# Optimization experiments

Measured on AMD Instinct MI355X. Metric: run time of the kernel, lower is better.

Reference implementation:

```python
import jax, jax.numpy as jnp
import numpy as np

N = 100000   # num nodes
E = 1000000  # num edges (avg degree 10)
F = 64       # feat_dim
H = 64       # hidden_dim
O = 16       # output_dim


def setup_inputs() -> dict:
    key = jax.random.key(0)
    ks = jax.random.split(key, 14)
    s = 0.05
    return {
        "real_feature": jax.random.normal(ks[0], (N, F), jnp.float32),
        "imag_feature": jax.random.normal(ks[1], (N, F), jnp.float32),
        "edge_weight_sym": jax.random.uniform(ks[2], (E,), jnp.float32),
        "exp_weight_q": jnp.float32(1.0),
        "edge_entropy": jax.random.uniform(ks[3], (E,), jnp.float32),
        "edge_cluster_coefficient": jax.random.uniform(ks[4], (E,), jnp.float32),
        "W1": jax.random.normal(ks[5], (H, F), jnp.float32) * s,
        "b1": jax.random.normal(ks[6], (H,), jnp.float32) * s,
        "W2": jax.random.normal(ks[7], (H, H), jnp.float32) * s,
        "b2": jax.random.normal(ks[8], (H,), jnp.float32) * s,
        "W3": jax.random.normal(ks[9], (O, 2 * H), jnp.float32) * s,
        "b3": jax.random.normal(ks[10], (O,), jnp.float32) * s,
        "row": jax.random.randint(ks[11], (E,), 0, N, jnp.int32),
        "col": jax.random.randint(ks[12], (E,), 0, N, jnp.int32),
    }


def reference(real_feature, imag_feature, edge_weight_sym, exp_weight_q,
              edge_entropy, edge_cluster_coefficient,
              W1, b1, W2, b2, W3, b3, row, col):
    # structure-encoded complex edge weights (soft_label is None branch)
    se = edge_entropy + edge_cluster_coefficient            # [E]
    phase = exp_weight_q * se
    wr = edge_weight_sym * jnp.cos(phase)                   # real adj values
    wi = edge_weight_sym * jnp.sin(phase)                   # imag adj values

    def spmm(w, x):
        # out[row] += w * x[col]  == torch.mm(sparse_coo(indices, w), x)
        return jax.ops.segment_sum(w[:, None] * x[col], row, num_segments=N)

    def layer(xr, xi, W, b):
        rr = spmm(wr, xr)   # real_adj @ real
        ii = spmm(wi, xi)   # imag_adj @ imag
        ir = spmm(wi, xr)   # imag_adj @ real
        ri = spmm(wr, xi)   # real_adj @ imag
        # fc(rr) - fc(ii): bias cancels; fc(ir) + fc(ri): bias doubles
        out_r = (rr - ii) @ W.T
        out_i = (ir + ri) @ W.T + 2.0 * b
        # ComReLU: ReLU applied to real and imag parts independently
        return jax.nn.relu(out_r), jax.nn.relu(out_i)

    r1, i1 = layer(real_feature, imag_feature, W1, b1)  # dropout=eval -> identity
    r2, i2 = layer(r1, i1, W2, b2)
    x = jnp.concatenate([r2, i2], axis=-1)              # [N, 2H]
    return x @ W3.T + b3                                # [N, O]
```

## Files before the change

### kernel.cpp

```cpp
#include <hip/hip_runtime.h>
#include <hip/hip_fp16.h>


typedef __attribute__((ext_vector_type(8))) _Float16 half8;
typedef __attribute__((ext_vector_type(4))) float f32x4;

#define LW 72
#define LW3 136
#define NBKTMAX 400
#define CAP 16

__device__ __forceinline__ unsigned short hbits(float f) {
  return __half_as_ushort(__float2half_rn(f));
}
__device__ __forceinline__ unsigned packh2(float a, float b) {
  return ((unsigned)hbits(b) << 16) | (unsigned)hbits(a);
}
__device__ __forceinline__ float2 unpackh2(unsigned u) {
  __half2 h = *reinterpret_cast<__half2*>(&u);
  return __half22float2(h);
}

__global__ void prep_k(const float4* __restrict__ xr, const float4* __restrict__ xi,
                       uint4* __restrict__ xc, int n4,
                       const int* __restrict__ row, int* __restrict__ cnt, int E) {
  int i = blockIdx.x * 256 + threadIdx.x;
  if (i < E) atomicAdd(&cnt[row[i]], 1);
  if (i < n4) {
    float4 r = xr[i], m = xi[i];
    xc[i] = make_uint4(packh2(r.x, m.x), packh2(r.y, m.y),
                       packh2(r.z, m.z), packh2(r.w, m.w));
  }
}

__global__ void offs_k(const int* __restrict__ cnt, int* __restrict__ offs,
                       int* __restrict__ total,
                       int* __restrict__ gcur, int N, int nch) {
  int ch = blockIdx.x * 4 + (threadIdx.x >> 6);
  if (ch >= nch) return;
  int lane = threadIdx.x & 63;
  int n0 = ch * 256 + lane * 4;
  int v0 = 0, v1 = 0, v2 = 0, v3 = 0;
  if (n0 + 3 < N) {
    int4 v = *(const int4*)&cnt[n0];
    v0 = v.x; v1 = v.y; v2 = v.z; v3 = v.w;
  } else {
    if (n0 + 0 < N) v0 = cnt[n0 + 0];
    if (n0 + 1 < N) v1 = cnt[n0 + 1];
    if (n0 + 2 < N) v2 = cnt[n0 + 2];
    if (n0 + 3 < N) v3 = cnt[n0 + 3];
  }
  int s = v0 + v1 + v2 + v3;
  int x = s;
#pragma unroll
  for (int d = 1; d < 64; d <<= 1) {
    int t = __shfl_up(x, d);
    if (lane >= d) x += t;
  }
  int excl = x - s;
  int wtot = __shfl(x, 63);
  int base = 0;
  if (lane == 63) base = atomicAdd(total, wtot);
  base = __shfl(base, 63);
  if (lane == 0) gcur[ch] = base;
  int e0 = base + excl;
  if (n0 + 0 < N) offs[n0 + 0] = e0;
  if (n0 + 1 < N) offs[n0 + 1] = e0 + v0;
  if (n0 + 2 < N) offs[n0 + 2] = e0 + v0 + v1;
  if (n0 + 3 < N) offs[n0 + 3] = e0 + v0 + v1 + v2;
}

__global__ void __launch_bounds__(256) bin_k(
    const int* __restrict__ row, const int* __restrict__ col,
    const float* __restrict__ wsym, const float* __restrict__ qp,
    const float* __restrict__ ent, const float* __restrict__ cc,
    int* __restrict__ gcur, uint2* __restrict__ tmp,
    int E, int nbkt, int ntiles) {
  __shared__ int lcnt[NBKTMAX];
  __shared__ int lgp[NBKTMAX];
  __shared__ uint2 lbuf[NBKTMAX * CAP];
  const float q = qp[0];
  for (int t = blockIdx.x; t < ntiles; t += gridDim.x) {
    for (int i = threadIdx.x; i < nbkt; i += 256) lcnt[i] = 0;
    __syncthreads();
    int base = t * 2048;
#pragma unroll
    for (int j = 0; j < 8; ++j) {
      int e = base + j * 256 + threadIdx.x;
      if (e < E) {
        float ph = q * (ent[e] + cc[e]);
        float s = __sinf(ph), c = __cosf(ph);
        float w = wsym[e];
        int r = row[e];
        uint2 rec = make_uint2((unsigned)col[e] | ((unsigned)(r & 255) << 24),
                               packh2(w * c, w * s));
        int b = r >> 8;
        int pos = atomicAdd(&lcnt[b], 1);
        if (pos < CAP) lbuf[b * CAP + pos] = rec;
        else {
          int gp = atomicAdd(&gcur[b], 1);
          tmp[gp] = rec;
        }
      }
    }
    __syncthreads();
    for (int b = threadIdx.x; b < nbkt; b += 256) {
      int c = lcnt[b];
      if (c > CAP) c = CAP;
      lgp[b] = (c > 0) ? atomicAdd(&gcur[b], c) : 0;
    }
    __syncthreads();
    int slots = nbkt * CAP;
    for (int i = threadIdx.x; i < slots; i += 256) {
      int b = i >> 4, j = i & (CAP - 1);
      int c = lcnt[b];
      if (c > CAP) c = CAP;
      if (j < c) tmp[lgp[b] + j] = lbuf[i];
    }
    __syncthreads();
  }
}

__global__ void __launch_bounds__(256) fine_k(
    const uint2* __restrict__ tmp, const int* __restrict__ offs,
    const int* __restrict__ cnt, uint2* __restrict__ crec, int N) {
  __shared__ int ls[256];
  __shared__ int fill[256];
  int first = blockIdx.x << 8;
  int nlast = first + 256;
  if (nlast > N) nlast = N;
  nlast -= 1;
  int beg = offs[first];
  int end = offs[nlast] + cnt[nlast];
  int tid = threadIdx.x;
  int n = first + tid;
  ls[tid] = (n <= nlast) ? (offs[n] - beg) : 0;
  fill[tid] = 0;
  __syncthreads();
  for (int i = beg + tid; i < end; i += 256) {
    uint2 r = tmp[i];
    int loc = (int)(r.x >> 24);
    unsigned c = r.x & 0xFFFFFFu;
    int pos = beg + ls[loc] + atomicAdd(&fill[loc], 1);
    crec[pos] = make_uint2(c | ((unsigned)(loc & 15) << 28), r.y);
  }
}

struct AccRI {
  f32x4 r[4], i[4];
};

__device__ __forceinline__ AccRI spmm_gemv(
    const unsigned* __restrict__ tbl,
    const int* __restrict__ offs, const int* __restrict__ cnt,
    const uint2* __restrict__ crec,
    const _Float16* __restrict__ sW,
    _Float16* __restrict__ s_ar, _Float16* __restrict__ s_ai,
    int n0, int N, int lane) {
  const int c16 = lane & 15, q16 = lane >> 4;
  int nlast = n0 + 15;
  if (nlast >= N) nlast = N - 1;
  int ebeg = __builtin_amdgcn_readfirstlane(offs[n0]);
  int eend = __builtin_amdgcn_readfirstlane(offs[nlast] + cnt[nlast]);
  int total = eend - ebeg;

  uint2 rA[16], rB[16];
  unsigned vA[16], vB[16];
  float ar = 0.f, ai = 0.f;
  int ni = 0;

#define LOADRECS(base_, recs_)                                        \
  do {                                                                \
    if ((base_) + 16 <= total) {                                      \
      _Pragma("unroll") for (int j = 0; j < 16; ++j)                  \
          (recs_)[j] = crec[ebeg + (base_) + j];                      \
    } else {                                                          \
      _Pragma("unroll") for (int j = 0; j < 16; ++j) {                \
        int idx_ = ((base_) + j < total) ? ebeg + (base_) + j : ebeg; \
        (recs_)[j] = crec[idx_];                                      \
      }                                                               \
    }                                                                 \
  } while (0)

#define ISSUEV(recs_, v_)                                                  \
  do {                                                                     \
    _Pragma("unroll") for (int j = 0; j < 16; ++j)                         \
        (v_)[j] = tbl[(unsigned)((recs_)[j].x & 0x0FFFFFFFu) * 64u + lane]; \
  } while (0)

#define FLUSHTO(nrel_)                      \
  while (ni < (nrel_)) {                    \
    s_ar[ni * LW + lane] = (_Float16)ar;    \
    s_ai[ni * LW + lane] = (_Float16)ai;    \
    ar = 0.f;                               \
    ai = 0.f;                               \
    ++ni;                                   \
  }

#define CONSUME(recs_, v_, base_)                               \
  do {                                                          \
    _Pragma("unroll") for (int j = 0; j < 16; ++j) {            \
      if ((base_) + j >= total) break;                          \
      int nrel_ = (recs_)[j].x >> 28;                           \
      FLUSHTO(nrel_);                                           \
      float2 val_ = unpackh2((v_)[j]);                          \
      float2 wv_ = unpackh2((recs_)[j].y);                      \
      ar = fmaf(wv_.x, val_.x, fmaf(-wv_.y, val_.y, ar));       \
      ai = fmaf(wv_.y, val_.x, fmaf(wv_.x, val_.y, ai));        \
    }                                                           \
  } while (0)

  int nbatch = (total + 15) >> 4;
  if (nbatch > 0) {
    LOADRECS(0, rA);
    ISSUEV(rA, vA);
    if (nbatch > 1) LOADRECS(16, rB);
    for (int b = 0; b < nbatch; b += 2) {
      if (b + 1 < nbatch) ISSUEV(rB, vB);
      CONSUME(rA, vA, b * 16);
      if (b + 2 < nbatch) LOADRECS((b + 2) * 16, rA);
      if (b + 1 < nbatch) {
        if (b + 2 < nbatch) ISSUEV(rA, vA);
        CONSUME(rB, vB, (b + 1) * 16);
        if (b + 3 < nbatch) LOADRECS((b + 3) * 16, rB);
      }
    }
  }
  FLUSHTO(16);
#undef LOADRECS
#undef ISSUEV
#undef FLUSHTO
#undef CONSUME

  half8 a_r[2], a_i[2];
#pragma unroll
  for (int ks = 0; ks < 2; ++ks) {
    int off = c16 * LW + ks * 32 + q16 * 8;
    a_r[ks] = *(const half8*)&s_ar[off];
    a_i[ks] = *(const half8*)&s_ai[off];
  }
  AccRI acc;
#pragma unroll
  for (int nt = 0; nt < 4; ++nt) {
    acc.r[nt] = (f32x4){0.f, 0.f, 0.f, 0.f};
    acc.i[nt] = (f32x4){0.f, 0.f, 0.f, 0.f};
  }
#pragma unroll
  for (int nt = 0; nt < 4; ++nt)
#pragma unroll
    for (int ks = 0; ks < 2; ++ks) {
      half8 b = *(const half8*)&sW[(nt * 16 + c16) * LW + ks * 32 + q16 * 8];
      acc.r[nt] = __builtin_amdgcn_mfma_f32_16x16x32_f16(a_r[ks], b, acc.r[nt], 0, 0, 0);
      acc.i[nt] = __builtin_amdgcn_mfma_f32_16x16x32_f16(a_i[ks], b, acc.i[nt], 0, 0, 0);
    }
  return acc;
}

__global__ void __launch_bounds__(512, 6) layer1_k(
    const unsigned* __restrict__ xc,
    const int* __restrict__ offs, const int* __restrict__ cnt,
    const uint2* __restrict__ crec,
    const float* __restrict__ W, const float* __restrict__ bias,
    unsigned* __restrict__ Hc, int N) {
  __shared__ __align__(16) _Float16 sW[64 * LW];
  __shared__ __align__(16) _Float16 s_act[8][2][16 * LW];
  for (int i = threadIdx.x; i < 64 * 64; i += 512)
    sW[(i >> 6) * LW + (i & 63)] = (_Float16)W[i];
  __syncthreads();
  const int w = threadIdx.x >> 6, lane = threadIdx.x & 63;
  const int c16 = lane & 15, q16 = lane >> 4;
  int n0 = (blockIdx.x * 8 + w) * 16;
  if (n0 >= N) return;
  float bl[4];
#pragma unroll
  for (int nt = 0; nt < 4; ++nt) bl[nt] = 2.f * bias[nt * 16 + c16];

  AccRI acc = spmm_gemv(xc, offs, cnt, crec, sW,
                        &s_act[w][0][0], &s_act[w][1][0], n0, N, lane);
#pragma unroll
  for (int nt = 0; nt < 4; ++nt)
#pragma unroll
    for (int r = 0; r < 4; ++r) {
      int node = n0 + q16 * 4 + r;
      if (node < N) {
        float hr = fmaxf(acc.r[nt][r], 0.f);
        float hi = fmaxf(acc.i[nt][r] + bl[nt], 0.f);
        Hc[(unsigned)node * 64u + nt * 16 + c16] = packh2(hr, hi);
      }
    }
}

__global__ void __launch_bounds__(512, 6) layer2_k(
    const unsigned* __restrict__ Hc,
    const int* __restrict__ offs, const int* __restrict__ cnt,
    const uint2* __restrict__ crec,
    const float* __restrict__ W2, const float* __restrict__ b2,
    const float* __restrict__ W3, const float* __restrict__ b3,
    float* __restrict__ out, int N) {
  __shared__ __align__(16) _Float16 sW[64 * LW];
  __shared__ __align__(16) _Float16 sW3p[16 * LW3];
  __shared__ __align__(16) _Float16 s_act[8][2][16 * LW];
  for (int i = threadIdx.x; i < 64 * 64; i += 512)
    sW[(i >> 6) * LW + (i & 63)] = (_Float16)W2[i];
  for (int i = threadIdx.x; i < 16 * 128; i += 512) {
    int o = i >> 7, kp = i & 127;
    sW3p[o * LW3 + kp] = (_Float16)W3[o * 128 + (kp >> 1) + 64 * (kp & 1)];
  }
  __syncthreads();
  const int w = threadIdx.x >> 6, lane = threadIdx.x & 63;
  const int c16 = lane & 15, q16 = lane >> 4;
  int n0 = (blockIdx.x * 8 + w) * 16;
  if (n0 >= N) return;
  float bl[4];
#pragma unroll
  for (int nt = 0; nt < 4; ++nt) bl[nt] = 2.f * b2[nt * 16 + c16];
  const float b3v = b3[c16];

  AccRI acc = spmm_gemv(Hc, offs, cnt, crec, sW,
                        &s_act[w][0][0], &s_act[w][1][0], n0, N, lane);

  unsigned* pb = (unsigned*)&s_act[w][0][0];
#pragma unroll
  for (int nt = 0; nt < 4; ++nt)
#pragma unroll
    for (int r = 0; r < 4; ++r) {
      float hr = fmaxf(acc.r[nt][r], 0.f);
      float hi = fmaxf(acc.i[nt][r] + bl[nt], 0.f);
      pb[(q16 * 4 + r) * 68 + nt * 16 + c16] = packh2(hr, hi);
    }
  f32x4 po = {0.f, 0.f, 0.f, 0.f};
#pragma unroll
  for (int ks = 0; ks < 4; ++ks) {
    half8 a = *(const half8*)((const _Float16*)pb + c16 * LW3 + ks * 32 + q16 * 8);
    half8 b = *(const half8*)&sW3p[c16 * LW3 + ks * 32 + q16 * 8];
    po = __builtin_amdgcn_mfma_f32_16x16x32_f16(a, b, po, 0, 0, 0);
  }
#pragma unroll
  for (int r = 0; r < 4; ++r) {
    int node = n0 + q16 * 4 + r;
    if (node < N) out[(unsigned)node * 16u + c16] = po[r] + b3v;
  }
}

extern "C" void kernel_launch(void* const* d_in, const int* in_sizes, int n_in,
                              void* d_out, int out_size, void* d_ws, size_t ws_size,
                              hipStream_t stream) {
  const float* xr   = (const float*)d_in[0];
  const float* xi   = (const float*)d_in[1];
  const float* wsym = (const float*)d_in[2];
  const float* qp   = (const float*)d_in[3];
  const float* ent  = (const float*)d_in[4];
  const float* cc   = (const float*)d_in[5];
  const float* W1   = (const float*)d_in[6];
  const float* b1   = (const float*)d_in[7];
  const float* W2   = (const float*)d_in[8];
  const float* b2   = (const float*)d_in[9];
  const float* W3   = (const float*)d_in[10];
  const float* b3   = (const float*)d_in[11];
  const int*   row  = (const int*)d_in[12];
  const int*   col  = (const int*)d_in[13];
  const int N = in_sizes[0] / 64;
  const int E = in_sizes[2];
  float* out = (float*)d_out;

  char* ws = (char*)d_ws;
  size_t off = 0;
  auto alloc = [&](size_t bytes) -> void* {
    void* p = ws + off;
    off += (bytes + 255) & ~(size_t)255;
    return p;
  };
  int*      cnt    = (int*)alloc((size_t)N * 4);
  int*      offs   = (int*)alloc((size_t)N * 4);
  int*      total  = (int*)alloc(256);
  int*      gcur   = (int*)alloc((size_t)NBKTMAX * 4);
  uint2*    crec   = (uint2*)alloc((size_t)E * 8);
  unsigned* xc     = (unsigned*)alloc((size_t)N * 64 * 4);
  unsigned* Hc     = (unsigned*)alloc((size_t)N * 64 * 4);
  uint2*    tmp    = (uint2*)Hc;

  hipMemsetAsync(cnt, 0, (size_t)N * 4, stream);
  hipMemsetAsync(total, 0, 256, stream);
  int n4 = N * 64 / 4;
  int npre = (n4 > E ? n4 : E);
  prep_k<<<(npre + 255) / 256, 256, 0, stream>>>((const float4*)xr, (const float4*)xi,
                                                 (uint4*)xc, n4, row, cnt, E);
  int nch = (N + 255) / 256;
  offs_k<<<(nch + 3) / 4, 256, 0, stream>>>(cnt, offs, total, gcur, N, nch);
  int ntiles = (E + 2047) / 2048;
  bin_k<<<ntiles, 256, 0, stream>>>(row, col, wsym, qp, ent, cc, gcur, tmp,
                                    E, nch, ntiles);
  fine_k<<<nch, 256, 0, stream>>>(tmp, offs, cnt, crec, N);
  int nb = (N + 127) / 128;
  layer1_k<<<nb, 512, 0, stream>>>(xc, offs, cnt, crec, W1, b1, Hc, N);
  layer2_k<<<nb, 512, 0, stream>>>(Hc, offs, cnt, crec, W2, b2, W3, b3, out, N);
}
```

Measured before the change: 198.6 us.

## Replace per-node global histogram with chunk histogram and in-block per-node counting

Per-node degree counting with global atomics is replaced by a shared-memory histogram over 256-node chunks plus a single-block chunk scan. Per-node offsets are now computed inside fine_k via a local count and block scan, and the CSR offsets array gains an N+1 sentinel so the cnt array goes away. The fp16 feature packing moves into bin_k, removing the prep kernel and the N-sized memset. This cuts global atomic contention and kernel count, at the cost of an extra pass over tmp in fine_k and a serial single-block scan.

```diff
diff --git a/kernel.cpp b/kernel.cpp
--- a/kernel.cpp
+++ b/kernel.cpp
@@ -21,61 +21,52 @@
   return __half22float2(h);
 }
 
-__global__ void prep_k(const float4* __restrict__ xr, const float4* __restrict__ xi,
-                       uint4* __restrict__ xc, int n4,
-                       const int* __restrict__ row, int* __restrict__ cnt, int E) {
-  int i = blockIdx.x * 256 + threadIdx.x;
-  if (i < E) atomicAdd(&cnt[row[i]], 1);
-  if (i < n4) {
-    float4 r = xr[i], m = xi[i];
-    xc[i] = make_uint4(packh2(r.x, m.x), packh2(r.y, m.y),
-                       packh2(r.z, m.z), packh2(r.w, m.w));
-  }
-}
-
-__global__ void offs_k(const int* __restrict__ cnt, int* __restrict__ offs,
-                       int* __restrict__ total,
-                       int* __restrict__ gcur, int N, int nch) {
-  int ch = blockIdx.x * 4 + (threadIdx.x >> 6);
-  if (ch >= nch) return;
-  int lane = threadIdx.x & 63;
-  int n0 = ch * 256 + lane * 4;
-  int v0 = 0, v1 = 0, v2 = 0, v3 = 0;
-  if (n0 + 3 < N) {
-    int4 v = *(const int4*)&cnt[n0];
-    v0 = v.x; v1 = v.y; v2 = v.z; v3 = v.w;
-  } else {
-    if (n0 + 0 < N) v0 = cnt[n0 + 0];
-    if (n0 + 1 < N) v1 = cnt[n0 + 1];
-    if (n0 + 2 < N) v2 = cnt[n0 + 2];
-    if (n0 + 3 < N) v3 = cnt[n0 + 3];
-  }
-  int s = v0 + v1 + v2 + v3;
-  int x = s;
-#pragma unroll
-  for (int d = 1; d < 64; d <<= 1) {
-    int t = __shfl_up(x, d);
-    if (lane >= d) x += t;
-  }
-  int excl = x - s;
-  int wtot = __shfl(x, 63);
-  int base = 0;
-  if (lane == 63) base = atomicAdd(total, wtot);
-  base = __shfl(base, 63);
-  if (lane == 0) gcur[ch] = base;
-  int e0 = base + excl;
-  if (n0 + 0 < N) offs[n0 + 0] = e0;
-  if (n0 + 1 < N) offs[n0 + 1] = e0 + v0;
-  if (n0 + 2 < N) offs[n0 + 2] = e0 + v0 + v1;
-  if (n0 + 3 < N) offs[n0 + 3] = e0 + v0 + v1 + v2;
+__global__ void hist_k(const int* __restrict__ row, int* __restrict__ chcnt,
+                       int E, int nch) {
+  __shared__ int h[NBKTMAX];
+  for (int i = threadIdx.x; i < nch; i += 256) h[i] = 0;
+  __syncthreads();
+  for (int e = blockIdx.x * 256 + threadIdx.x; e < E; e += gridDim.x * 256)
+    atomicAdd(&h[row[e] >> 8], 1);
+  __syncthreads();
+  for (int i = threadIdx.x; i < nch; i += 256)
+    if (h[i]) atomicAdd(&chcnt[i], h[i]);
+}
+
+__global__ void cscan_k(const int* __restrict__ chcnt, int* __restrict__ chbase,
+                        int* __restrict__ gcur, int nch, int E) {
+  __shared__ int buf[512];
+  int t = threadIdx.x;
+  int v = (t < nch) ? chcnt[t] : 0;
+  buf[t] = v;
+  __syncthreads();
+  for (int d = 1; d < 512; d <<= 1) {
+    int y = (t >= d) ? buf[t - d] : 0;
+    __syncthreads();
+    buf[t] += y;
+    __syncthreads();
+  }
+  int excl = buf[t] - v;
+  if (t < nch) {
+    chbase[t] = excl;
+    gcur[t] = excl;
+  }
+  if (t == nch) chbase[nch] = E;
 }
 
 __global__ void __launch_bounds__(256) bin_k(
+    const float4* __restrict__ xr, const float4* __restrict__ xi,
+    uint4* __restrict__ xc, int n4,
     const int* __restrict__ row, const int* __restrict__ col,
     const float* __restrict__ wsym, const float* __restrict__ qp,
     const float* __restrict__ ent, const float* __restrict__ cc,
     int* __restrict__ gcur, uint2* __restrict__ tmp,
     int E, int nbkt, int ntiles) {
+  for (int i = blockIdx.x * 256 + threadIdx.x; i < n4; i += gridDim.x * 256) {
+    float4 r = xr[i], m = xi[i];
+    xc[i] = make_uint4(packh2(r.x, m.x), packh2(r.y, m.y),
+                       packh2(r.z, m.z), packh2(r.w, m.w));
+  }
   __shared__ int lcnt[NBKTMAX];
   __shared__ int lgp[NBKTMAX];
   __shared__ uint2 lbuf[NBKTMAX * CAP];
@@ -122,20 +113,37 @@
 }
 
 __global__ void __launch_bounds__(256) fine_k(
-    const uint2* __restrict__ tmp, const int* __restrict__ offs,
-    const int* __restrict__ cnt, uint2* __restrict__ crec, int N) {
+    const uint2* __restrict__ tmp, const int* __restrict__ chbase,
+    int* __restrict__ offs, uint2* __restrict__ crec, int N) {
+  __shared__ int cntl[256];
   __shared__ int ls[256];
   __shared__ int fill[256];
-  int first = blockIdx.x << 8;
-  int nlast = first + 256;
-  if (nlast > N) nlast = N;
-  nlast -= 1;
-  int beg = offs[first];
-  int end = offs[nlast] + cnt[nlast];
+  __shared__ int buf[256];
   int tid = threadIdx.x;
+  int ch = blockIdx.x;
+  int first = ch << 8;
+  int beg = chbase[ch];
+  int end = chbase[ch + 1];
+  cntl[tid] = 0;
+  fill[tid] = 0;
+  __syncthreads();
+  for (int i = beg + tid; i < end; i += 256)
+    atomicAdd(&cntl[tmp[i].x >> 24], 1);
+  __syncthreads();
+  int v = cntl[tid];
+  buf[tid] = v;
+  __syncthreads();
+  for (int d = 1; d < 256; d <<= 1) {
+    int y = (tid >= d) ? buf[tid - d] : 0;
+    __syncthreads();
+    buf[tid] += y;
+    __syncthreads();
+  }
+  int excl = buf[tid] - v;
+  ls[tid] = excl;
   int n = first + tid;
-  ls[tid] = (n <= nlast) ? (offs[n] - beg) : 0;
-  fill[tid] = 0;
+  if (n < N) offs[n] = beg + excl;
+  if (tid == 0 && ch == gridDim.x - 1) offs[N] = end;
   __syncthreads();
   for (int i = beg + tid; i < end; i += 256) {
     uint2 r = tmp[i];
@@ -152,16 +160,16 @@
 
 __device__ __forceinline__ AccRI spmm_gemv(
     const unsigned* __restrict__ tbl,
-    const int* __restrict__ offs, const int* __restrict__ cnt,
+    const int* __restrict__ offs,
     const uint2* __restrict__ crec,
     const _Float16* __restrict__ sW,
     _Float16* __restrict__ s_ar, _Float16* __restrict__ s_ai,
     int n0, int N, int lane) {
   const int c16 = lane & 15, q16 = lane >> 4;
-  int nlast = n0 + 15;
-  if (nlast >= N) nlast = N - 1;
+  int nend = n0 + 16;
+  if (nend > N) nend = N;
   int ebeg = __builtin_amdgcn_readfirstlane(offs[n0]);
-  int eend = __builtin_amdgcn_readfirstlane(offs[nlast] + cnt[nlast]);
+  int eend = __builtin_amdgcn_readfirstlane(offs[nend]);
   int total = eend - ebeg;
 
   uint2 rA[16], rB[16];
@@ -258,7 +266,7 @@
 
 __global__ void __launch_bounds__(512, 6) layer1_k(
     const unsigned* __restrict__ xc,
-    const int* __restrict__ offs, const int* __restrict__ cnt,
+    const int* __restrict__ offs,
     const uint2* __restrict__ crec,
     const float* __restrict__ W, const float* __restrict__ bias,
     unsigned* __restrict__ Hc, int N) {
@@ -275,7 +283,7 @@
 #pragma unroll
   for (int nt = 0; nt < 4; ++nt) bl[nt] = 2.f * bias[nt * 16 + c16];
 
-  AccRI acc = spmm_gemv(xc, offs, cnt, crec, sW,
+  AccRI acc = spmm_gemv(xc, offs, crec, sW,
                         &s_act[w][0][0], &s_act[w][1][0], n0, N, lane);
 #pragma unroll
   for (int nt = 0; nt < 4; ++nt)
@@ -292,7 +300,7 @@
 
 __global__ void __launch_bounds__(512, 6) layer2_k(
     const unsigned* __restrict__ Hc,
-    const int* __restrict__ offs, const int* __restrict__ cnt,
+    const int* __restrict__ offs,
     const uint2* __restrict__ crec,
     const float* __restrict__ W2, const float* __restrict__ b2,
     const float* __restrict__ W3, const float* __restrict__ b3,
@@ -316,7 +324,7 @@
   for (int nt = 0; nt < 4; ++nt) bl[nt] = 2.f * b2[nt * 16 + c16];
   const float b3v = b3[c16];
 
-  AccRI acc = spmm_gemv(Hc, offs, cnt, crec, sW,
+  AccRI acc = spmm_gemv(Hc, offs, crec, sW,
                         &s_act[w][0][0], &s_act[w][1][0], n0, N, lane);
 
   unsigned* pb = (unsigned*)&s_act[w][0][0];
@@ -370,28 +378,26 @@
     off += (bytes + 255) & ~(size_t)255;
     return p;
   };
-  int*      cnt    = (int*)alloc((size_t)N * 4);
-  int*      offs   = (int*)alloc((size_t)N * 4);
-  int*      total  = (int*)alloc(256);
+  int*      chcnt  = (int*)alloc((size_t)NBKTMAX * 4);
+  int*      chbase = (int*)alloc((size_t)(NBKTMAX + 1) * 4);
   int*      gcur   = (int*)alloc((size_t)NBKTMAX * 4);
+  int*      offs   = (int*)alloc((size_t)(N + 1) * 4);
   uint2*    crec   = (uint2*)alloc((size_t)E * 8);
   unsigned* xc     = (unsigned*)alloc((size_t)N * 64 * 4);
   unsigned* Hc     = (unsigned*)alloc((size_t)N * 64 * 4);
   uint2*    tmp    = (uint2*)Hc;
 
-  hipMemsetAsync(cnt, 0, (size_t)N * 4, stream);
-  hipMemsetAsync(total, 0, 256, stream);
+  hipMemsetAsync(chcnt, 0, (size_t)NBKTMAX * 4, stream);
+  int nch = (N + 255) / 256;
+  int ntiles = (E + 2047) / 2048;
+  hist_k<<<ntiles, 256, 0, stream>>>(row, chcnt, E, nch);
+  cscan_k<<<1, 512, 0, stream>>>(chcnt, chbase, gcur, nch, E);
   int n4 = N * 64 / 4;
-  int npre = (n4 > E ? n4 : E);
-  prep_k<<<(npre + 255) / 256, 256, 0, stream>>>((const float4*)xr, (const float4*)xi,
-                                                 (uint4*)xc, n4, row, cnt, E);
-  int nch = (N + 255) / 256;
-  offs_k<<<(nch + 3) / 4, 256, 0, stream>>>(cnt, offs, total, gcur, N, nch);
-  int ntiles = (E + 2047) / 2048;
-  bin_k<<<ntiles, 256, 0, stream>>>(row, col, wsym, qp, ent, cc, gcur, tmp,
-                                    E, nch, ntiles);
-  fine_k<<<nch, 256, 0, stream>>>(tmp, offs, cnt, crec, N);
+  bin_k<<<ntiles, 256, 0, stream>>>((const float4*)xr, (const float4*)xi,
+                                    (uint4*)xc, n4, row, col, wsym, qp, ent, cc,
+                                    gcur, tmp, E, nch, ntiles);
+  fine_k<<<nch, 256, 0, stream>>>(tmp, chbase, offs, crec, N);
   int nb = (N + 127) / 128;
-  layer1_k<<<nb, 512, 0, stream>>>(xc, offs, cnt, crec, W1, b1, Hc, N);
-  layer2_k<<<nb, 512, 0, stream>>>(Hc, offs, cnt, crec, W2, b2, W3, b3, out, N);
-}
+  layer1_k<<<nb, 512, 0, stream>>>(xc, offs, crec, W1, b1, Hc, N);
+  layer2_k<<<nb, 512, 0, stream>>>(Hc, offs, crec, W2, b2, W3, b3, out, N);
+}
```

After: 171.4 us. 1.16x faster.
